# Kernel optimization log

Hardware: AMD Instinct MI355X
Metric: run time of the kernel (lower is better)

## Reference

```python
import jax, jax.numpy as jnp
import numpy as np

B, L, D_IN, D_OUT = 4, 1024, 2048, 2048
H, G = 32, 8            # num_heads, num_kv_groups
HD = D_OUT // H         # head_dim = 64
R = H // G              # group_size = 4


def setup_inputs() -> dict:
    key = jax.random.key(0)
    ks = jax.random.split(key, 7)
    s = 0.02
    return {
        "query": jax.random.normal(ks[0], (B, L, D_IN), jnp.float32),
        "key": jax.random.normal(ks[1], (B, L, D_IN), jnp.float32),
        "value": jax.random.normal(ks[2], (B, L, D_IN), jnp.float32),
        "Wq": jax.random.normal(ks[3], (D_IN, D_OUT), jnp.float32) * s,
        "Wk": jax.random.normal(ks[4], (D_IN, G * HD), jnp.float32) * s,
        "Wv": jax.random.normal(ks[5], (D_IN, G * HD), jnp.float32) * s,
        "Wo": jax.random.normal(ks[6], (D_OUT, D_OUT), jnp.float32) * s,
        # causal mask: positions where mask==True are set to -inf (original uses attn_mask == 1)
        "attn_mask": jnp.triu(jnp.ones((L, L), dtype=bool), k=1),
    }


def reference(query, key, value, Wq, Wk, Wv, Wo, attn_mask):
    b, t, _ = query.shape
    # projections (Linear, no bias)
    q = (query @ Wq).reshape(b, t, G, R, HD)      # head h = g*R + r matches repeat_interleave ordering
    k = (key @ Wk).reshape(b, -1, G, HD)
    v = (value @ Wv).reshape(b, -1, G, HD)
    # NOTE: original code applies NO 1/sqrt(head_dim) scaling — kept faithful.
    # scores: (b, g, r, t, s); KV broadcast over r instead of repeat_interleave
    scores = jnp.einsum('btgrd,bsgd->bgrts', q, k)
    scores = jnp.where(attn_mask[None, None, None, :, :], -jnp.inf, scores)
    weights = jax.nn.softmax(scores, axis=-1)     # dropout p=0.0 -> identity
    ctx = jnp.einsum('bgrts,bsgd->btgrd', weights, v).reshape(b, t, D_OUT)
    attn_output = ctx @ Wo
    attn_output_weights = weights.reshape(b * H, t, -1)  # (b n) t s
    return attn_output, attn_output_weights
```

## Files before the change

### kernel.cpp

```cpp
#include <hip/hip_runtime.h>
#include <math.h>

typedef _Float16 f16;
typedef __attribute__((ext_vector_type(8))) _Float16 f16x8;
typedef __attribute__((ext_vector_type(4))) _Float16 f16x4;
typedef __attribute__((ext_vector_type(4))) float f32x4;
typedef unsigned int u32;

#define MFMA16(a, b, c) __builtin_amdgcn_mfma_f32_16x16x32_f16(a, b, c, 0, 0, 0)

__device__ __forceinline__ void gload16(const void* g, void* l) {
  __builtin_amdgcn_global_load_lds((const __attribute__((address_space(1))) u32*)g,
                                   (__attribute__((address_space(3))) u32*)l, 16, 0, 0);
}

__global__ __launch_bounds__(256) void prep_kernel(
    const float* __restrict__ q, const float* __restrict__ k, const float* __restrict__ v,
    f16* __restrict__ qh, f16* __restrict__ kh, f16* __restrict__ vh,
    const float* __restrict__ Wq, const float* __restrict__ Wk,
    const float* __restrict__ Wv, const float* __restrict__ Wo,
    f16* __restrict__ WqT, f16* __restrict__ WkT,
    f16* __restrict__ WvT, f16* __restrict__ WoT) {
  __shared__ f16 tile[64][66];
  const int bx = blockIdx.x;
  const int t = threadIdx.x;
  if (bx < 24576) {
    const int sel = bx >> 13;
    const float* in = (sel == 0) ? q : (sel == 1) ? k : v;
    f16* out = (sel == 0) ? qh : (sel == 1) ? kh : vh;
    const int i = (bx & 8191) * 1024 + t * 4;
    float4 vv = *(const float4*)(in + i);
    f16x4 h;
    h[0] = (f16)vv.x; h[1] = (f16)vv.y; h[2] = (f16)vv.z; h[3] = (f16)vv.w;
    *(f16x4*)(out + i) = h;
    return;
  }
  int id = bx - 24576;
  const float* in;
  f16* out;
  int K, N;
  if (id < 1024)      { in = Wq; out = WqT; K = 2048; N = 2048; }
  else if (id < 1280) { in = Wk; out = WkT; K = 2048; N = 512;  id -= 1024; }
  else if (id < 1536) { in = Wv; out = WvT; K = 2048; N = 512;  id -= 1280; }
  else                { in = Wo; out = WoT; K = 2048; N = 2048; id -= 1536; }
  const int ntn = N >> 6;
  const int tk = (id / ntn) * 64, tn = (id % ntn) * 64;
#pragma unroll
  for (int i = 0; i < 16; i++) {
    int idx = i * 256 + t;
    int r = idx >> 6, c = idx & 63;
    tile[c][r] = (f16)in[(size_t)(tk + r) * N + tn + c];
  }
  __syncthreads();
#pragma unroll
  for (int i = 0; i < 16; i++) {
    int idx = i * 256 + t;
    int r = idx >> 6, c = idx & 63;
    out[(size_t)(tn + r) * K + tk + c] = tile[r][c];
  }
}

template <bool F32OUT>
__device__ __forceinline__ void gemm_body(const f16* __restrict__ Ap,
                                          const f16* __restrict__ Btp,
                                          void* __restrict__ Cp,
                                          int m0, int n0, int N, int K, int vmode) {
  const int tid = threadIdx.x, lane = tid & 63, wid = tid >> 6;
  const int lg = lane >> 4, lr = lane & 15;
  const int wr = (wid >> 1) << 6, wc = (wid & 1) << 6;
  __shared__ f16 As[2][128 * 64];
  __shared__ f16 Bs[2][128 * 64];
  auto stage = [&](const f16* Gp, f16* Ls, int row0, int k0) {
#pragma unroll
    for (int c = 0; c < 4; c++) {
      int u = c * 256 + tid;
      int row = u >> 3, slot = u & 7;
      int gs = slot ^ (row & 7);
      gload16(Gp + (size_t)(row0 + row) * K + k0 + gs * 8,
              Ls + (c * 256 + wid * 64) * 8);
    }
  };
  f32x4 acc[4][4] = {};
  const int nk = K >> 6;
  stage(Ap, As[0], m0, 0);
  stage(Btp, Bs[0], n0, 0);
  for (int k = 0; k < nk; k++) {
    const int cb = k & 1;
    __builtin_amdgcn_s_barrier();
    __builtin_amdgcn_sched_barrier(0);
    if (k + 1 < nk) {
      stage(Ap, As[cb ^ 1], m0, (k + 1) << 6);
      stage(Btp, Bs[cb ^ 1], n0, (k + 1) << 6);
      __builtin_amdgcn_sched_barrier(0);
      asm volatile("s_waitcnt vmcnt(8)" ::: "memory");
    } else {
      __builtin_amdgcn_sched_barrier(0);
      asm volatile("s_waitcnt vmcnt(0)" ::: "memory");
    }
    __builtin_amdgcn_s_barrier();
    __builtin_amdgcn_sched_barrier(0);
    asm volatile("" ::: "memory");
#pragma unroll
    for (int kk = 0; kk < 2; kk++) {
      f16x8 af[4], bf[4];
#pragma unroll
      for (int i = 0; i < 4; i++) {
        int row = wr + i * 16 + lr;
        int sl = (kk * 4 + lg) ^ (row & 7);
        af[i] = *(const f16x8*)&As[cb][row * 64 + sl * 8];
      }
#pragma unroll
      for (int i = 0; i < 4; i++) {
        int row = wc + i * 16 + lr;
        int sl = (kk * 4 + lg) ^ (row & 7);
        bf[i] = *(const f16x8*)&Bs[cb][row * 64 + sl * 8];
      }
#pragma unroll
      for (int i = 0; i < 4; i++)
#pragma unroll
        for (int j = 0; j < 4; j++)
          acc[i][j] = MFMA16(af[i], bf[j], acc[i][j]);
    }
  }
  if (F32OUT) {
    float* C = (float*)Cp;
#pragma unroll
    for (int i = 0; i < 4; i++)
#pragma unroll
      for (int j = 0; j < 4; j++)
#pragma unroll
        for (int rg = 0; rg < 4; rg++) {
          int row = m0 + wr + i * 16 + lg * 4 + rg;
          int col = n0 + wc + j * 16 + lr;
          C[(size_t)row * N + col] = acc[i][j][rg];
        }
  } else if (vmode) {
    f16* C = (f16*)Cp;
#pragma unroll
    for (int i = 0; i < 4; i++)
#pragma unroll
      for (int j = 0; j < 4; j++)
#pragma unroll
        for (int rg = 0; rg < 4; rg++) {
          int row = m0 + wr + i * 16 + lg * 4 + rg;
          int col = n0 + wc + j * 16 + lr;
          C[((size_t)(row >> 10) * 512 + col) * 1024 + (row & 1023)] = (f16)acc[i][j][rg];
        }
  } else {
    f16* C = (f16*)Cp;
#pragma unroll
    for (int i = 0; i < 4; i++)
#pragma unroll
      for (int j = 0; j < 4; j++)
#pragma unroll
        for (int rg = 0; rg < 4; rg++) {
          int row = m0 + wr + i * 16 + lg * 4 + rg;
          int col = n0 + wc + j * 16 + lr;
          C[(size_t)row * N + col] = (f16)acc[i][j][rg];
        }
  }
}

__global__ __launch_bounds__(256) void gemm_proj(
    const f16* __restrict__ qh, const f16* __restrict__ WqT, f16* __restrict__ Qp,
    const f16* __restrict__ kh, const f16* __restrict__ WkT, f16* __restrict__ Kpj,
    const f16* __restrict__ vh, const f16* __restrict__ WvT, f16* __restrict__ VTp,
    float* __restrict__ wout) {
  const int bx = blockIdx.x;
  const int grp = bx / 5, rem = bx % 5;
  if (rem >= 3) {
    const int zid = grp * 2 + (rem - 3);
#pragma unroll
    for (int ci = 0; ci < 4; ci++) {
      const int c = zid * 4 + ci;
      const int bh = c >> 4, k = c & 15;
      if (k == 15) continue;
      const int cols0 = (k + 1) << 6;
      const int nc4 = (1024 - cols0) >> 2;
      float* base = wout + (size_t)bh * 1024 * 1024 + (size_t)(k << 6) * 1024 + cols0;
      f32x4 z = {};
      for (int r = 0; r < 64; r++) {
        float* rp = base + (size_t)r * 1024;
        for (int c4 = (int)threadIdx.x; c4 < nc4; c4 += 256)
          __builtin_nontemporal_store(z, (f32x4*)(rp + c4 * 4));
      }
    }
    return;
  }
  const int gid = grp * 3 + rem;
  const f16 *Ap, *Btp;
  f16* Cp;
  int N, nsh, vmode, tile;
  if (gid < 512)      { Ap = qh; Btp = WqT; Cp = Qp;  N = 2048; nsh = 4; vmode = 0; tile = gid; }
  else if (gid < 640) { Ap = kh; Btp = WkT; Cp = Kpj; N = 512;  nsh = 2; vmode = 0; tile = gid - 512; }
  else                { Ap = vh; Btp = WvT; Cp = VTp; N = 512;  nsh = 2; vmode = 1; tile = gid - 640; }
  const int m0 = (tile >> nsh) << 7, n0 = (tile & ((1 << nsh) - 1)) << 7;
  gemm_body<false>(Ap, Btp, (void*)Cp, m0, n0, N, 2048, vmode);
}

__global__ __launch_bounds__(256) void gemm_out(
    const f16* __restrict__ Ap, const f16* __restrict__ Btp, float* __restrict__ Cp) {
  const int tile = blockIdx.x;
  const int m0 = (tile >> 4) << 7, n0 = (tile & 15) << 7;
  gemm_body<true>(Ap, Btp, (void*)Cp, m0, n0, 2048, 2048, 0);
}

__global__ __launch_bounds__(256) void attn_kernel(
    const f16* __restrict__ Qp, const f16* __restrict__ Kp, const f16* __restrict__ VTp,
    float* __restrict__ Wout, f16* __restrict__ Ctx) {
  __shared__ f16 Kt[2][64 * 64];
  __shared__ f16 Vt[2][64 * 64];
  __shared__ f16 Wt[4][16 * 64];
  const int bx = (blockIdx.x & 7) * 128 + (blockIdx.x >> 3);
  const int qt = bx & 31, g = (bx >> 5) & 7, b = bx >> 8;
  const int tid = threadIdx.x, lane = tid & 63, wid = tid >> 6;
  const int lg = lane >> 4, lr = lane & 15;
  const int h = g * 4 + wid;
  const int q0 = qt * 32;
  const int st_max = (q0 + 31) >> 6;
  const float S0 = 12.0f;

  f16x8 aq[2][2];
#pragma unroll
  for (int mi = 0; mi < 2; mi++)
#pragma unroll
    for (int kk = 0; kk < 2; kk++)
      aq[mi][kk] = *(const f16x8*)(Qp + (size_t)(b * 1024 + q0 + mi * 16 + lr) * 2048 +
                                   h * 64 + kk * 32 + lg * 8);

  float l_[2][4] = {};

  auto stageK = [&](int st, int buf) {
#pragma unroll
    for (int c = 0; c < 2; c++) {
      int u = c * 256 + tid;
      int row = u >> 3, slot = u & 7;
      int gs = slot ^ (row & 7);
      gload16(Kp + (size_t)(b * 1024 + st * 64 + row) * 512 + g * 64 + gs * 8,
              &Kt[buf][(c * 256 + wid * 64) * 8]);
    }
  };
  auto stageV = [&](int st, int buf) {
#pragma unroll
    for (int c = 0; c < 2; c++) {
      int u = c * 256 + tid;
      int row = u >> 3, slot = u & 7;
      int gs = slot ^ (row & 7);
      gload16(VTp + ((size_t)b * 512 + g * 64 + row) * 1024 + st * 64 + gs * 8,
              &Vt[buf][(c * 256 + wid * 64) * 8]);
    }
  };

  int cur = 0;
  stageK(0, 0);
  for (int st = 0; st <= st_max; st++) {
    __syncthreads();
    if (st < st_max) {
      stageK(st + 1, cur ^ 1);
    } else {
      stageK(0, cur ^ 1);
      stageV(0, cur ^ 1);
    }
    f16x8 bk[4][2];
#pragma unroll
    for (int ni = 0; ni < 4; ni++)
#pragma unroll
      for (int kk = 0; kk < 2; kk++) {
        int row = ni * 16 + lr;
        int sl = (kk * 4 + lg) ^ (row & 7);
        bk[ni][kk] = *(const f16x8*)&Kt[cur][row * 64 + sl * 8];
      }
#pragma unroll
    for (int mi = 0; mi < 2; mi++) {
      f32x4 s[4];
#pragma unroll
      for (int ni = 0; ni < 4; ni++) {
        f32x4 z = {};
        z = MFMA16(aq[mi][0], bk[ni][0], z);
        z = MFMA16(aq[mi][1], bk[ni][1], z);
        s[ni] = z;
      }
      if (st == st_max) {
#pragma unroll
        for (int ni = 0; ni < 4; ni++)
#pragma unroll
          for (int rg = 0; rg < 4; rg++)
            if (st * 64 + ni * 16 + lr > q0 + mi * 16 + lg * 4 + rg) s[ni][rg] = -INFINITY;
      }
#pragma unroll
      for (int rg = 0; rg < 4; rg++) {
        float rs = __expf(s[0][rg] - S0) + __expf(s[1][rg] - S0) +
                   __expf(s[2][rg] - S0) + __expf(s[3][rg] - S0);
        rs += __shfl_xor(rs, 1);
        rs += __shfl_xor(rs, 2);
        rs += __shfl_xor(rs, 4);
        rs += __shfl_xor(rs, 8);
        l_[mi][rg] += rs;
      }
    }
    cur ^= 1;
  }
#pragma unroll
  for (int i = 0; i < 2; i++)
#pragma unroll
    for (int j = 0; j < 4; j++) l_[i][j] = 1.0f / l_[i][j];

  f32x4 o[2][4] = {};
  for (int st = 0; st <= st_max; st++) {
    __syncthreads();
    if (st < st_max) {
      stageK(st + 1, cur ^ 1);
      stageV(st + 1, cur ^ 1);
    }
    f16x8 bk[4][2];
#pragma unroll
    for (int ni = 0; ni < 4; ni++)
#pragma unroll
      for (int kk = 0; kk < 2; kk++) {
        int row = ni * 16 + lr;
        int sl = (kk * 4 + lg) ^ (row & 7);
        bk[ni][kk] = *(const f16x8*)&Kt[cur][row * 64 + sl * 8];
      }
#pragma unroll
    for (int mi = 0; mi < 2; mi++) {
#pragma unroll
      for (int ni = 0; ni < 4; ni++) {
        f32x4 z = {};
        z = MFMA16(aq[mi][0], bk[ni][0], z);
        z = MFMA16(aq[mi][1], bk[ni][1], z);
#pragma unroll
        for (int rg = 0; rg < 4; rg++) {
          float sv = z[rg];
          if (st == st_max && (st * 64 + ni * 16 + lr > q0 + mi * 16 + lg * 4 + rg))
            sv = -INFINITY;
          float w = __expf(sv - S0) * l_[mi][rg];
          int rowl = mi * 16 + lg * 4 + rg;
          __builtin_nontemporal_store(
              w, &Wout[((size_t)(b * 32 + h) * 1024 + q0 + rowl) * 1024 +
                       st * 64 + ni * 16 + lr]);
          int r16 = lg * 4 + rg;
          int sl2 = (2 * ni + (lr >> 3)) ^ (r16 & 7);
          Wt[wid][r16 * 64 + sl2 * 8 + (lr & 7)] = (f16)w;
        }
      }
#pragma unroll
      for (int kk = 0; kk < 2; kk++) {
        f16x8 aw, bv[4];
        {
          int sl = (kk * 4 + lg) ^ (lr & 7);
          aw = *(const f16x8*)&Wt[wid][lr * 64 + sl * 8];
        }
#pragma unroll
        for (int j = 0; j < 4; j++) {
          int rv = j * 16 + lr;
          int sl = (kk * 4 + lg) ^ (rv & 7);
          bv[j] = *(const f16x8*)&Vt[cur][rv * 64 + sl * 8];
        }
#pragma unroll
        for (int j = 0; j < 4; j++)
          o[mi][j] = MFMA16(aw, bv[j], o[mi][j]);
      }
    }
    cur ^= 1;
  }

#pragma unroll
  for (int i = 0; i < 2; i++)
#pragma unroll
    for (int j = 0; j < 4; j++)
#pragma unroll
      for (int rg = 0; rg < 4; rg++)
        Ctx[(size_t)(b * 1024 + q0 + i * 16 + lg * 4 + rg) * 2048 +
            h * 64 + j * 16 + lr] = (f16)o[i][j][rg];
}

extern "C" void kernel_launch(void* const* d_in, const int* in_sizes, int n_in,
                              void* d_out, int out_size, void* d_ws, size_t ws_size,
                              hipStream_t stream) {
  const float* query = (const float*)d_in[0];
  const float* key   = (const float*)d_in[1];
  const float* value = (const float*)d_in[2];
  const float* Wq    = (const float*)d_in[3];
  const float* Wk    = (const float*)d_in[4];
  const float* Wv    = (const float*)d_in[5];
  const float* Wo    = (const float*)d_in[6];

  float* out0 = (float*)d_out;
  float* wout = out0 + (size_t)4 * 1024 * 2048;

  char* ws = (char*)d_ws;
  size_t off = 0;
  auto alloc = [&](size_t bytes) {
    char* p = ws + off;
    off += (bytes + 255) & ~(size_t)255;
    return p;
  };
  const size_t NT = 4096;
  f16* qh  = (f16*)alloc(NT * 2048 * 2);
  f16* kh  = (f16*)alloc(NT * 2048 * 2);
  f16* vh  = (f16*)alloc(NT * 2048 * 2);
  f16* WqT = (f16*)alloc((size_t)2048 * 2048 * 2);
  f16* WkT = (f16*)alloc((size_t)512 * 2048 * 2);
  f16* WvT = (f16*)alloc((size_t)512 * 2048 * 2);
  f16* WoT = (f16*)alloc((size_t)2048 * 2048 * 2);
  f16* Qp  = (f16*)alloc(NT * 2048 * 2);
  f16* Kpj = (f16*)alloc(NT * 512 * 2);
  f16* VTp = (f16*)alloc(NT * 512 * 2);
  f16* ctx = (f16*)alloc(NT * 2048 * 2);
  (void)ws_size;

  hipLaunchKernelGGL(prep_kernel, dim3(27136), dim3(256), 0, stream,
                     query, key, value, qh, kh, vh,
                     Wq, Wk, Wv, Wo, WqT, WkT, WvT, WoT);
  hipLaunchKernelGGL(gemm_proj, dim3(1280), dim3(256), 0, stream,
                     qh, WqT, Qp, kh, WkT, Kpj, vh, WvT, VTp, wout);
  hipLaunchKernelGGL(attn_kernel, dim3(1024), dim3(256), 0, stream,
                     Qp, Kpj, VTp, wout, ctx);
  hipLaunchKernelGGL(gemm_out, dim3(512), dim3(256), 0, stream, ctx, WoT, out0);
  (void)in_sizes; (void)n_in; (void)out_size;
}
```

Baseline: 330.4 us.

## Pair causal query tiles per block to balance attention work and share K/V loads

Each attention block now handles two 32-row query tiles, kpair and 31-kpair, so every block does about the same amount of causal work, and the grid is halved to 512 blocks. The K and V tiles staged in LDS are reused by both query tiles while the low tile is still active. The cost is more registers (doubled Q fragments, accumulators and row sums), which may lower occupancy, and fewer blocks to spread across the CUs.

```diff
diff --git a/kernel.cpp b/kernel.cpp
--- a/kernel.cpp
+++ b/kernel.cpp
@@ -211,24 +211,28 @@
   __shared__ f16 Kt[2][64 * 64];
   __shared__ f16 Vt[2][64 * 64];
   __shared__ f16 Wt[4][16 * 64];
-  const int bx = (blockIdx.x & 7) * 128 + (blockIdx.x >> 3);
-  const int qt = bx & 31, g = (bx >> 5) & 7, b = bx >> 8;
+  const int id = (blockIdx.x & 7) * 64 + (blockIdx.x >> 3);
+  const int kpair = id & 15, g = (id >> 4) & 7, b = id >> 7;
   const int tid = threadIdx.x, lane = tid & 63, wid = tid >> 6;
   const int lg = lane >> 4, lr = lane & 15;
   const int h = g * 4 + wid;
-  const int q0 = qt * 32;
-  const int st_max = (q0 + 31) >> 6;
+  const int q0s[2] = {kpair * 32, (31 - kpair) * 32};
+  const int stm0 = (q0s[0] + 31) >> 6;
+  const int st_hi = (q0s[1] + 31) >> 6;
   const float S0 = 12.0f;
 
-  f16x8 aq[2][2];
-#pragma unroll
-  for (int mi = 0; mi < 2; mi++)
-#pragma unroll
-    for (int kk = 0; kk < 2; kk++)
-      aq[mi][kk] = *(const f16x8*)(Qp + (size_t)(b * 1024 + q0 + mi * 16 + lr) * 2048 +
-                                   h * 64 + kk * 32 + lg * 8);
-
-  float l_[2][4] = {};
+  f16x8 aq[2][2][2];
+#pragma unroll
+  for (int qi = 0; qi < 2; qi++)
+#pragma unroll
+    for (int mi = 0; mi < 2; mi++)
+#pragma unroll
+      for (int kk = 0; kk < 2; kk++)
+        aq[qi][mi][kk] = *(const f16x8*)(Qp +
+            (size_t)(b * 1024 + q0s[qi] + mi * 16 + lr) * 2048 +
+            h * 64 + kk * 32 + lg * 8);
+
+  float l_[2][2][4] = {};
 
   auto stageK = [&](int st, int buf) {
 #pragma unroll
@@ -253,9 +257,9 @@
 
   int cur = 0;
   stageK(0, 0);
-  for (int st = 0; st <= st_max; st++) {
+  for (int st = 0; st <= st_hi; st++) {
     __syncthreads();
-    if (st < st_max) {
+    if (st < st_hi) {
       stageK(st + 1, cur ^ 1);
     } else {
       stageK(0, cur ^ 1);
@@ -271,44 +275,53 @@
         bk[ni][kk] = *(const f16x8*)&Kt[cur][row * 64 + sl * 8];
       }
 #pragma unroll
-    for (int mi = 0; mi < 2; mi++) {
-      f32x4 s[4];
-#pragma unroll
-      for (int ni = 0; ni < 4; ni++) {
-        f32x4 z = {};
-        z = MFMA16(aq[mi][0], bk[ni][0], z);
-        z = MFMA16(aq[mi][1], bk[ni][1], z);
-        s[ni] = z;
-      }
-      if (st == st_max) {
-#pragma unroll
-        for (int ni = 0; ni < 4; ni++)
-#pragma unroll
-          for (int rg = 0; rg < 4; rg++)
-            if (st * 64 + ni * 16 + lr > q0 + mi * 16 + lg * 4 + rg) s[ni][rg] = -INFINITY;
-      }
-#pragma unroll
-      for (int rg = 0; rg < 4; rg++) {
-        float rs = __expf(s[0][rg] - S0) + __expf(s[1][rg] - S0) +
-                   __expf(s[2][rg] - S0) + __expf(s[3][rg] - S0);
-        rs += __shfl_xor(rs, 1);
-        rs += __shfl_xor(rs, 2);
-        rs += __shfl_xor(rs, 4);
-        rs += __shfl_xor(rs, 8);
-        l_[mi][rg] += rs;
+    for (int qi = 0; qi < 2; qi++) {
+      if (qi == 0 && st > stm0) continue;
+      const int q0 = q0s[qi];
+      const int stq = qi ? st_hi : stm0;
+#pragma unroll
+      for (int mi = 0; mi < 2; mi++) {
+        f32x4 s[4];
+#pragma unroll
+        for (int ni = 0; ni < 4; ni++) {
+          f32x4 z = {};
+          z = MFMA16(aq[qi][mi][0], bk[ni][0], z);
+          z = MFMA16(aq[qi][mi][1], bk[ni][1], z);
+          s[ni] = z;
+        }
+        if (st == stq) {
+#pragma unroll
+          for (int ni = 0; ni < 4; ni++)
+#pragma unroll
+            for (int rg = 0; rg < 4; rg++)
+              if (st * 64 + ni * 16 + lr > q0 + mi * 16 + lg * 4 + rg)
+                s[ni][rg] = -INFINITY;
+        }
+#pragma unroll
+        for (int rg = 0; rg < 4; rg++) {
+          float rs = __expf(s[0][rg] - S0) + __expf(s[1][rg] - S0) +
+                     __expf(s[2][rg] - S0) + __expf(s[3][rg] - S0);
+          rs += __shfl_xor(rs, 1);
+          rs += __shfl_xor(rs, 2);
+          rs += __shfl_xor(rs, 4);
+          rs += __shfl_xor(rs, 8);
+          l_[qi][mi][rg] += rs;
+        }
       }
     }
     cur ^= 1;
   }
 #pragma unroll
-  for (int i = 0; i < 2; i++)
-#pragma unroll
-    for (int j = 0; j < 4; j++) l_[i][j] = 1.0f / l_[i][j];
-
-  f32x4 o[2][4] = {};
-  for (int st = 0; st <= st_max; st++) {
+  for (int qi = 0; qi < 2; qi++)
+#pragma unroll
+    for (int i = 0; i < 2; i++)
+#pragma unroll
+      for (int j = 0; j < 4; j++) l_[qi][i][j] = 1.0f / l_[qi][i][j];
+
+  f32x4 o[2][2][4] = {};
+  for (int st = 0; st <= st_hi; st++) {
     __syncthreads();
-    if (st < st_max) {
+    if (st < st_hi) {
       stageK(st + 1, cur ^ 1);
       stageV(st + 1, cur ^ 1);
     }
@@ -322,56 +335,64 @@
         bk[ni][kk] = *(const f16x8*)&Kt[cur][row * 64 + sl * 8];
       }
 #pragma unroll
-    for (int mi = 0; mi < 2; mi++) {
-#pragma unroll
-      for (int ni = 0; ni < 4; ni++) {
-        f32x4 z = {};
-        z = MFMA16(aq[mi][0], bk[ni][0], z);
-        z = MFMA16(aq[mi][1], bk[ni][1], z);
-#pragma unroll
-        for (int rg = 0; rg < 4; rg++) {
-          float sv = z[rg];
-          if (st == st_max && (st * 64 + ni * 16 + lr > q0 + mi * 16 + lg * 4 + rg))
-            sv = -INFINITY;
-          float w = __expf(sv - S0) * l_[mi][rg];
-          int rowl = mi * 16 + lg * 4 + rg;
-          __builtin_nontemporal_store(
-              w, &Wout[((size_t)(b * 32 + h) * 1024 + q0 + rowl) * 1024 +
-                       st * 64 + ni * 16 + lr]);
-          int r16 = lg * 4 + rg;
-          int sl2 = (2 * ni + (lr >> 3)) ^ (r16 & 7);
-          Wt[wid][r16 * 64 + sl2 * 8 + (lr & 7)] = (f16)w;
-        }
-      }
-#pragma unroll
-      for (int kk = 0; kk < 2; kk++) {
-        f16x8 aw, bv[4];
-        {
-          int sl = (kk * 4 + lg) ^ (lr & 7);
-          aw = *(const f16x8*)&Wt[wid][lr * 64 + sl * 8];
-        }
-#pragma unroll
-        for (int j = 0; j < 4; j++) {
-          int rv = j * 16 + lr;
-          int sl = (kk * 4 + lg) ^ (rv & 7);
-          bv[j] = *(const f16x8*)&Vt[cur][rv * 64 + sl * 8];
-        }
-#pragma unroll
-        for (int j = 0; j < 4; j++)
-          o[mi][j] = MFMA16(aw, bv[j], o[mi][j]);
+    for (int qi = 0; qi < 2; qi++) {
+      if (qi == 0 && st > stm0) continue;
+      const int q0 = q0s[qi];
+      const int stq = qi ? st_hi : stm0;
+#pragma unroll
+      for (int mi = 0; mi < 2; mi++) {
+#pragma unroll
+        for (int ni = 0; ni < 4; ni++) {
+          f32x4 z = {};
+          z = MFMA16(aq[qi][mi][0], bk[ni][0], z);
+          z = MFMA16(aq[qi][mi][1], bk[ni][1], z);
+#pragma unroll
+          for (int rg = 0; rg < 4; rg++) {
+            float sv = z[rg];
+            if (st == stq && (st * 64 + ni * 16 + lr > q0 + mi * 16 + lg * 4 + rg))
+              sv = -INFINITY;
+            float w = __expf(sv - S0) * l_[qi][mi][rg];
+            int rowl = mi * 16 + lg * 4 + rg;
+            __builtin_nontemporal_store(
+                w, &Wout[((size_t)(b * 32 + h) * 1024 + q0 + rowl) * 1024 +
+                         st * 64 + ni * 16 + lr]);
+            int r16 = lg * 4 + rg;
+            int sl2 = (2 * ni + (lr >> 3)) ^ (r16 & 7);
+            Wt[wid][r16 * 64 + sl2 * 8 + (lr & 7)] = (f16)w;
+          }
+        }
+#pragma unroll
+        for (int kk = 0; kk < 2; kk++) {
+          f16x8 aw, bv[4];
+          {
+            int sl = (kk * 4 + lg) ^ (lr & 7);
+            aw = *(const f16x8*)&Wt[wid][lr * 64 + sl * 8];
+          }
+#pragma unroll
+          for (int j = 0; j < 4; j++) {
+            int rv = j * 16 + lr;
+            int sl = (kk * 4 + lg) ^ (rv & 7);
+            bv[j] = *(const f16x8*)&Vt[cur][rv * 64 + sl * 8];
+          }
+#pragma unroll
+          for (int j = 0; j < 4; j++)
+            o[qi][mi][j] = MFMA16(aw, bv[j], o[qi][mi][j]);
+        }
       }
     }
     cur ^= 1;
   }
 
 #pragma unroll
-  for (int i = 0; i < 2; i++)
-#pragma unroll
-    for (int j = 0; j < 4; j++)
-#pragma unroll
-      for (int rg = 0; rg < 4; rg++)
-        Ctx[(size_t)(b * 1024 + q0 + i * 16 + lg * 4 + rg) * 2048 +
-            h * 64 + j * 16 + lr] = (f16)o[i][j][rg];
+  for (int qi = 0; qi < 2; qi++)
+#pragma unroll
+    for (int i = 0; i < 2; i++)
+#pragma unroll
+      for (int j = 0; j < 4; j++)
+#pragma unroll
+        for (int rg = 0; rg < 4; rg++)
+          Ctx[(size_t)(b * 1024 + q0s[qi] + i * 16 + lg * 4 + rg) * 2048 +
+              h * 64 + j * 16 + lr] = (f16)o[qi][i][j][rg];
 }
 
 extern "C" void kernel_launch(void* const* d_in, const int* in_sizes, int n_in,
@@ -414,7 +435,7 @@
                      Wq, Wk, Wv, Wo, WqT, WkT, WvT, WoT);
   hipLaunchKernelGGL(gemm_proj, dim3(1280), dim3(256), 0, stream,
                      qh, WqT, Qp, kh, WkT, Kpj, vh, WvT, VTp, wout);
-  hipLaunchKernelGGL(attn_kernel, dim3(1024), dim3(256), 0, stream,
+  hipLaunchKernelGGL(attn_kernel, dim3(512), dim3(256), 0, stream,
                      Qp, Kpj, VTp, wout, ctx);
   hipLaunchKernelGGL(gemm_out, dim3(512), dim3(256), 0, stream, ctx, WoT, out0);
   (void)in_sizes; (void)n_in; (void)out_size;
```

Result: slower. 347.2 us (+5.1%).
